# Optimization experiments

Hardware: AMD Instinct MI355X
Metric: run time of the kernel (lower is better)

The kernel has to match this reference:

```python
import jax, jax.numpy as jnp
import numpy as np

B, T, H, I = 128, 1024, 512, 64
DT, TAU, NOISE_VAR = 1.0, 10.0, 0.1


def setup_inputs() -> dict:
    key = jax.random.key(0)
    k1, k2, k3, k4 = jax.random.split(key, 4)
    x = jax.random.normal(k1, (B, T, I), dtype=jnp.float32)
    # W_in: rows have unit-ish norm in the original init; normal/sqrt(I) is equivalent scale
    W_in = jax.random.normal(k2, (H, I), dtype=jnp.float32) / np.float32(np.sqrt(I))
    # W_hidden: randn/sqrt(H) then spectral-radius normalized; /sqrt(H) gives radius ~1
    W_hidden = jax.random.normal(k3, (H, H), dtype=jnp.float32) / np.float32(np.sqrt(H))
    # noise drawn inside forward in the original; materialized here: N(0, noise_var)
    sigma = jax.random.normal(k4, (H, T, B), dtype=jnp.float32) * np.float32(NOISE_VAR)
    h0 = jnp.zeros((H, B), dtype=jnp.float32)
    return {"x": x, "W_in": W_in, "W_hidden": W_hidden, "sigma": sigma, "h0": h0}


def reference(x, W_in, W_hidden, sigma, h0):
    c1 = jnp.float32(1.0 - DT / TAU)
    c2 = jnp.float32(DT / TAU)
    # precomputed input projection: [T, H, B] (scan carries over leading T axis)
    w_input = jnp.einsum("hi,bti->thb", W_in, x)
    sig = jnp.transpose(sigma, (1, 0, 2))  # [T, H, B]

    def step(h, inp):
        w_in_t, s_t = inp
        w_h = W_hidden @ jax.nn.sigmoid(h)          # [H, B]
        h_new = c1 * h + c2 * (w_in_t + w_h + s_t)  # leaky integration
        return h_new, h_new.T                        # emit [B, H]

    h_last, out_tbh = jax.lax.scan(step, h0, (w_input, sig))
    out = jnp.transpose(out_tbh, (1, 0, 2))  # [B, T, H]
    return out, h_last
```

## Files before the change

### kernel.cpp

```cpp
#include <hip/hip_runtime.h>
#include <stdint.h>

#define B_  128
#define T_  1024
#define H_  512
#define I_  64
#define TB_ 131072

typedef _Float16 half2_t __attribute__((ext_vector_type(2)));

union U32H2 { uint32_t u; half2_t h; };
union U16H  { uint16_t u; _Float16 h; };

static __device__ __forceinline__ half2_t u2h(uint32_t u){ U32H2 x; x.u=u; return x.h; }
static __device__ __forceinline__ uint32_t h2u(half2_t h){ U32H2 x; x.h=h; return x.u; }

#if defined(__has_builtin)
#if __has_builtin(__builtin_amdgcn_fdot2)
#define HAVE_FDOT2 1
#endif
#endif

static __device__ __forceinline__ float fdot2f(half2_t a, half2_t b, float c){
#ifdef HAVE_FDOT2
    return __builtin_amdgcn_fdot2(a, b, c, false);
#else
    return c + (float)a[0]*(float)b[0] + (float)a[1]*(float)b[1];
#endif
}

__global__ __launch_bounds__(256) void k_wingemm(const float* __restrict__ x,
                                                 const float* __restrict__ Win,
                                                 uint32_t* __restrict__ r2)
{
    __shared__ float As[128*65];
    __shared__ float Ws[64*65];
    const int t   = blockIdx.x;
    const int j0  = blockIdx.y * 64;
    const int tid = threadIdx.x;

#pragma unroll
    for (int k = 0; k < 8; k++){
        int qid = k*256 + tid;
        int row = qid >> 4;
        int qq  = qid & 15;
        float4 v = *(const float4*)(x + ((size_t)row*T_ + t)*I_ + qq*4);
        float* d = As + row*65 + qq*4;
        d[0]=v.x; d[1]=v.y; d[2]=v.z; d[3]=v.w;
    }
#pragma unroll
    for (int k = 0; k < 4; k++){
        int qid = k*256 + tid;
        int row = qid >> 4;
        int qq  = qid & 15;
        float4 v = *(const float4*)(Win + (size_t)(j0+row)*I_ + qq*4);
        float* d = Ws + row*65 + qq*4;
        d[0]=v.x; d[1]=v.y; d[2]=v.z; d[3]=v.w;
    }
    __syncthreads();

    const int tj = tid & 15;
    const int tb = tid >> 4;

    float acc[8][2][2];
#pragma unroll
    for (int bb=0; bb<8; bb++)
#pragma unroll
        for (int jj=0; jj<2; jj++){ acc[bb][jj][0]=0.f; acc[bb][jj][1]=0.f; }

#pragma unroll 4
    for (int i = 0; i < 64; i++){
        float a[8];
#pragma unroll
        for (int bb=0; bb<8; bb++) a[bb] = As[(tb + 16*bb)*65 + i];
        float wv[2][2];
#pragma unroll
        for (int jj=0; jj<2; jj++){
            wv[jj][0] = Ws[(2*tj + 32*jj    )*65 + i];
            wv[jj][1] = Ws[(2*tj + 32*jj + 1)*65 + i];
        }
#pragma unroll
        for (int bb=0; bb<8; bb++)
#pragma unroll
            for (int jj=0; jj<2; jj++){
                acc[bb][jj][0] += a[bb]*wv[jj][0];
                acc[bb][jj][1] += a[bb]*wv[jj][1];
            }
    }

#pragma unroll
    for (int bb=0; bb<8; bb++){
        int mi = t*128 + tb + 16*bb;
#pragma unroll
        for (int jj=0; jj<2; jj++){
            half2_t hv; hv[0]=(_Float16)acc[bb][jj][0]; hv[1]=(_Float16)acc[bb][jj][1];
            r2[(size_t)mi*256 + (j0>>1) + tj + 16*jj] = h2u(hv);
        }
    }
}

static __device__ __forceinline__ uint32_t addpair(uint32_t u, float a0, float a1){
    half2_t h = u2h(u);
    half2_t o; o[0]=(_Float16)((float)h[0] + a0); o[1]=(_Float16)((float)h[1] + a1);
    return h2u(o);
}

__global__ __launch_bounds__(256) void k_addsig(const float* __restrict__ sigma,
                                                uint32_t* __restrict__ r2)
{
    __shared__ float Ss[64*256];
    const int mi0 = blockIdx.x * 256;
    const int j0  = blockIdx.y * 64;
    const int tid = threadIdx.x;

#pragma unroll
    for (int k = 0; k < 16; k++){
        int qid = k*256 + tid;
        int row = qid >> 6;
        int qq  = qid & 63;
        float4 v = *(const float4*)(sigma + (size_t)(j0+row)*TB_ + mi0 + qq*4);
        *(float4*)(Ss + row*256 + qq*4) = v;
    }
    __syncthreads();

    const int mi = mi0 + tid;
    uint32_t* rr = r2 + (size_t)mi*256 + (j0>>1);
#pragma unroll
    for (int k = 0; k < 8; k++){
        uint4 q = *(uint4*)(rr + 4*k);
        q.x = addpair(q.x, Ss[(8*k+0)*256+tid], Ss[(8*k+1)*256+tid]);
        q.y = addpair(q.y, Ss[(8*k+2)*256+tid], Ss[(8*k+3)*256+tid]);
        q.z = addpair(q.z, Ss[(8*k+4)*256+tid], Ss[(8*k+5)*256+tid]);
        q.w = addpair(q.w, Ss[(8*k+6)*256+tid], Ss[(8*k+7)*256+tid]);
        *(uint4*)(rr + 4*k) = q;
    }
}

__global__ __launch_bounds__(512, 2) void k_rnn(const float* __restrict__ Wh,
                                                const float* __restrict__ Win,
                                                const float* __restrict__ x,
                                                const float* __restrict__ sigma,
                                                const float* __restrict__ h0,
                                                const uint16_t* __restrict__ r16,
                                                float* __restrict__ out,
                                                int use_r)
{
    extern __shared__ char smem[];
    uint32_t*  WL  = (uint32_t*)smem;
    float*     par = (float*)(smem + 131072);
    _Float16*  sb  = (_Float16*)(smem + 147456);

    const int b = blockIdx.x;
    const int t = threadIdx.x;
    const int w = t >> 6;
    const int l = t & 63;
    const int j = t;
    const int phase = (l & 15) << 2;

    half2_t wreg[6][32];
#pragma unroll
    for (int m = 0; m < 8; m++){
        const int row = l + 64*m;
        const float4* wr = (const float4*)(Wh + (size_t)row*H_ + (w << 6));
#pragma unroll
        for (int q = 0; q < 16; q++){
            float4 v = wr[q];
            half2_t a; a[0]=(_Float16)v.x; a[1]=(_Float16)v.y;
            half2_t c; c[0]=(_Float16)v.z; c[1]=(_Float16)v.w;
            int pp = 2*q;
            if (m < 6){
                wreg[m][pp]   = a;
                wreg[m][pp+1] = c;
            } else {
                int base = (m-6)*32;
                WL[t*64 + ((base + pp     + phase) & 63)] = h2u(a);
                WL[t*64 + ((base + pp + 1 + phase) & 63)] = h2u(c);
            }
        }
    }

    float h = h0[(size_t)j*B_ + b];
    const uint32_t* WLt = WL + t*64;
    const uint32_t* sbu = (const uint32_t*)sb;
    float* outp = out + (size_t)b*T_*H_ + j;
    const uint16_t* rp = r16 + (size_t)b*H_ + j;

    for (int ts = 0; ts < T_; ts++){
        uint16_t ru = 0;
        if (use_r) ru = rp[(size_t)ts * 65536];

        float e = __expf(-h);
        float s = 1.0f / (1.0f + e);
        sb[j] = (_Float16)s;
        __syncthreads();

        float p[8];
#pragma unroll
        for (int m = 0; m < 8; m++) p[m] = 0.f;

#pragma unroll
        for (int c = 0; c < 8; c++){
            uint4 sq = *(const uint4*)(sbu + (w << 5) + (c << 2));
            half2_t s0=u2h(sq.x), s1=u2h(sq.y), s2=u2h(sq.z), s3=u2h(sq.w);
            uint4 q6 = *(const uint4*)(WLt + ((4*c      + phase) & 63));
            uint4 q7 = *(const uint4*)(WLt + ((32 + 4*c + phase) & 63));
#pragma unroll
            for (int m = 0; m < 6; m++){
                p[m] = fdot2f(wreg[m][4*c+0], s0, p[m]);
                p[m] = fdot2f(wreg[m][4*c+1], s1, p[m]);
                p[m] = fdot2f(wreg[m][4*c+2], s2, p[m]);
                p[m] = fdot2f(wreg[m][4*c+3], s3, p[m]);
            }
            p[6] = fdot2f(u2h(q6.x), s0, p[6]);
            p[6] = fdot2f(u2h(q6.y), s1, p[6]);
            p[6] = fdot2f(u2h(q6.z), s2, p[6]);
            p[6] = fdot2f(u2h(q6.w), s3, p[6]);
            p[7] = fdot2f(u2h(q7.x), s0, p[7]);
            p[7] = fdot2f(u2h(q7.y), s1, p[7]);
            p[7] = fdot2f(u2h(q7.z), s2, p[7]);
            p[7] = fdot2f(u2h(q7.w), s3, p[7]);
        }

#pragma unroll
        for (int m = 0; m < 8; m++) par[(w << 9) + l + (m << 6)] = p[m];
        __syncthreads();

        float P = par[j] + par[j+512] + par[j+1024] + par[j+1536]
                + par[j+2048] + par[j+2560] + par[j+3072] + par[j+3584];

        float rv;
        if (use_r){
            U16H cv; cv.u = ru;
            rv = (float)cv.h;
        } else {
            float acc = 0.f;
            const float4* wir = (const float4*)(Win + (size_t)j*I_);
            const float4* xr  = (const float4*)(x + ((size_t)b*T_ + ts)*I_);
#pragma unroll
            for (int q = 0; q < 16; q++){
                float4 a = wir[q]; float4 xx = xr[q];
                acc += a.x*xx.x + a.y*xx.y + a.z*xx.z + a.w*xx.w;
            }
            rv = acc + sigma[((size_t)j << 17) + (ts << 7) + b];
        }

        h = 0.9f*h + 0.1f*(P + rv);
        outp[(size_t)ts * H_] = h;
    }

    out[(size_t)B_*T_*H_ + (size_t)j*B_ + b] = h;
}

extern "C" void kernel_launch(void* const* d_in, const int* in_sizes, int n_in,
                              void* d_out, int out_size, void* d_ws, size_t ws_size,
                              hipStream_t stream)
{
    const float* x     = (const float*)d_in[0];
    const float* Win   = (const float*)d_in[1];
    const float* Wh    = (const float*)d_in[2];
    const float* sigma = (const float*)d_in[3];
    const float* h0    = (const float*)d_in[4];
    float* out = (float*)d_out;

    const size_t r_bytes = (size_t)TB_ * H_ * 2;
    const int use_r = (ws_size >= r_bytes) ? 1 : 0;

    if (use_r){
        k_wingemm<<<dim3(T_, 8), 256, 0, stream>>>(x, Win, (uint32_t*)d_ws);
        k_addsig <<<dim3(TB_/256, 8), 256, 0, stream>>>(sigma, (uint32_t*)d_ws);
    }

    const int lds_bytes = 131072 + 16384 + 1024;
    (void)hipFuncSetAttribute((const void*)k_rnn,
                              hipFuncAttributeMaxDynamicSharedMemorySize, lds_bytes);
    k_rnn<<<B_, 512, lds_bytes, stream>>>(Wh, Win, x, sigma, h0,
                                          (const uint16_t*)d_ws, out, use_r);
}
```

Before: 2.525 ms.

## Fuse input projection and noise add into one prep kernel; vectorize RNN weight registers

Replaces the separate W_in GEMM kernel and sigma-add kernel with a single k_prep kernel per timestep. It computes all 512 hidden outputs in two 256-wide chunks, adds sigma from global memory and writes the fp16 result once, which removes a full read-modify-write pass over the workspace. The recurrent kernel's register-resident weights move from a 2D half2 array to six 32-wide uint32 vectors and use waves_per_eu attributes, to encourage the compiler to keep them in VGPRs without spilling. The sigma reads in k_prep are strided per thread, which may coalesce poorly, and the RNN loop itself stays the dominant serial cost.

Result: slower. 3.504 ms (+38.7%).

```diff
diff --git a/kernel.cpp b/kernel.cpp
--- a/kernel.cpp
+++ b/kernel.cpp
@@ -8,6 +8,7 @@
 #define TB_ 131072
 
 typedef _Float16 half2_t __attribute__((ext_vector_type(2)));
+typedef uint32_t u32v32  __attribute__((ext_vector_type(32)));
 
 union U32H2 { uint32_t u; half2_t h; };
 union U16H  { uint16_t u; _Float16 h; };
@@ -29,121 +30,96 @@
 #endif
 }
 
-__global__ __launch_bounds__(256) void k_wingemm(const float* __restrict__ x,
-                                                 const float* __restrict__ Win,
-                                                 uint32_t* __restrict__ r2)
+#define PADA 68
+
+__global__ __attribute__((amdgpu_flat_work_group_size(512,512)))
+void k_prep(const float* __restrict__ x, const float* __restrict__ Win,
+            const float* __restrict__ sigma, uint32_t* __restrict__ r2)
 {
-    __shared__ float As[128*65];
-    __shared__ float Ws[64*65];
+    extern __shared__ float smemA[];
+    float* As = smemA;
+    float* Ws = smemA + 128*PADA;
+
     const int t   = blockIdx.x;
-    const int j0  = blockIdx.y * 64;
     const int tid = threadIdx.x;
-
-#pragma unroll
-    for (int k = 0; k < 8; k++){
-        int qid = k*256 + tid;
-        int row = qid >> 4;
-        int qq  = qid & 15;
+    const int tm  = tid & 31;
+    const int tg  = tid >> 5;
+
+#pragma unroll
+    for (int k = 0; k < 4; k++){
+        int qid = k*512 + tid;
+        int row = qid >> 4, qq = qid & 15;
         float4 v = *(const float4*)(x + ((size_t)row*T_ + t)*I_ + qq*4);
-        float* d = As + row*65 + qq*4;
-        d[0]=v.x; d[1]=v.y; d[2]=v.z; d[3]=v.w;
-    }
-#pragma unroll
-    for (int k = 0; k < 4; k++){
-        int qid = k*256 + tid;
-        int row = qid >> 4;
-        int qq  = qid & 15;
-        float4 v = *(const float4*)(Win + (size_t)(j0+row)*I_ + qq*4);
-        float* d = Ws + row*65 + qq*4;
-        d[0]=v.x; d[1]=v.y; d[2]=v.z; d[3]=v.w;
-    }
-    __syncthreads();
-
-    const int tj = tid & 15;
-    const int tb = tid >> 4;
-
-    float acc[8][2][2];
-#pragma unroll
-    for (int bb=0; bb<8; bb++)
-#pragma unroll
-        for (int jj=0; jj<2; jj++){ acc[bb][jj][0]=0.f; acc[bb][jj][1]=0.f; }
-
-#pragma unroll 4
-    for (int i = 0; i < 64; i++){
-        float a[8];
-#pragma unroll
-        for (int bb=0; bb<8; bb++) a[bb] = As[(tb + 16*bb)*65 + i];
-        float wv[2][2];
-#pragma unroll
-        for (int jj=0; jj<2; jj++){
-            wv[jj][0] = Ws[(2*tj + 32*jj    )*65 + i];
-            wv[jj][1] = Ws[(2*tj + 32*jj + 1)*65 + i];
-        }
-#pragma unroll
-        for (int bb=0; bb<8; bb++)
-#pragma unroll
-            for (int jj=0; jj<2; jj++){
-                acc[bb][jj][0] += a[bb]*wv[jj][0];
-                acc[bb][jj][1] += a[bb]*wv[jj][1];
+        *(float4*)(As + row*PADA + qq*4) = v;
+    }
+
+    for (int ch = 0; ch < 2; ch++){
+        const int j0 = ch*256;
+        __syncthreads();
+#pragma unroll
+        for (int k = 0; k < 8; k++){
+            int qid = k*512 + tid;
+            int row = qid >> 4, qq = qid & 15;
+            float4 v = *(const float4*)(Win + (size_t)(j0+row)*I_ + qq*4);
+            *(float4*)(Ws + row*PADA + qq*4) = v;
+        }
+        __syncthreads();
+
+        float acc[4][16];
+#pragma unroll
+        for (int rr=0;rr<4;rr++)
+#pragma unroll
+            for (int jj=0;jj<16;jj++) acc[rr][jj] = 0.f;
+
+#pragma unroll
+        for (int ic = 0; ic < 16; ic++){
+            float4 a4[4];
+#pragma unroll
+            for (int rr=0;rr<4;rr++)
+                a4[rr] = *(const float4*)(As + (size_t)(tm+32*rr)*PADA + ic*4);
+#pragma unroll
+            for (int jj=0;jj<16;jj++){
+                float4 wv = *(const float4*)(Ws + (size_t)(tg*16+jj)*PADA + ic*4);
+#pragma unroll
+                for (int rr=0;rr<4;rr++)
+                    acc[rr][jj] += a4[rr].x*wv.x + a4[rr].y*wv.y
+                                 + a4[rr].z*wv.z + a4[rr].w*wv.w;
             }
-    }
-
-#pragma unroll
-    for (int bb=0; bb<8; bb++){
-        int mi = t*128 + tb + 16*bb;
-#pragma unroll
-        for (int jj=0; jj<2; jj++){
-            half2_t hv; hv[0]=(_Float16)acc[bb][jj][0]; hv[1]=(_Float16)acc[bb][jj][1];
-            r2[(size_t)mi*256 + (j0>>1) + tj + 16*jj] = h2u(hv);
-        }
-    }
-}
-
-static __device__ __forceinline__ uint32_t addpair(uint32_t u, float a0, float a1){
-    half2_t h = u2h(u);
-    half2_t o; o[0]=(_Float16)((float)h[0] + a0); o[1]=(_Float16)((float)h[1] + a1);
-    return h2u(o);
-}
-
-__global__ __launch_bounds__(256) void k_addsig(const float* __restrict__ sigma,
-                                                uint32_t* __restrict__ r2)
-{
-    __shared__ float Ss[64*256];
-    const int mi0 = blockIdx.x * 256;
-    const int j0  = blockIdx.y * 64;
-    const int tid = threadIdx.x;
-
-#pragma unroll
-    for (int k = 0; k < 16; k++){
-        int qid = k*256 + tid;
-        int row = qid >> 6;
-        int qq  = qid & 63;
-        float4 v = *(const float4*)(sigma + (size_t)(j0+row)*TB_ + mi0 + qq*4);
-        *(float4*)(Ss + row*256 + qq*4) = v;
-    }
-    __syncthreads();
-
-    const int mi = mi0 + tid;
-    uint32_t* rr = r2 + (size_t)mi*256 + (j0>>1);
-#pragma unroll
-    for (int k = 0; k < 8; k++){
-        uint4 q = *(uint4*)(rr + 4*k);
-        q.x = addpair(q.x, Ss[(8*k+0)*256+tid], Ss[(8*k+1)*256+tid]);
-        q.y = addpair(q.y, Ss[(8*k+2)*256+tid], Ss[(8*k+3)*256+tid]);
-        q.z = addpair(q.z, Ss[(8*k+4)*256+tid], Ss[(8*k+5)*256+tid]);
-        q.w = addpair(q.w, Ss[(8*k+6)*256+tid], Ss[(8*k+7)*256+tid]);
-        *(uint4*)(rr + 4*k) = q;
-    }
-}
-
-__global__ __launch_bounds__(512, 2) void k_rnn(const float* __restrict__ Wh,
-                                                const float* __restrict__ Win,
-                                                const float* __restrict__ x,
-                                                const float* __restrict__ sigma,
-                                                const float* __restrict__ h0,
-                                                const uint16_t* __restrict__ r16,
-                                                float* __restrict__ out,
-                                                int use_r)
+        }
+
+#pragma unroll
+        for (int rr=0; rr<4; rr++){
+            const size_t mi = (size_t)t*128 + tm + 32*rr;
+            const float* sp = sigma + (size_t)(j0 + tg*16)*TB_ + mi;
+            uint32_t ou[8];
+#pragma unroll
+            for (int k2=0;k2<8;k2++){
+                float sA = sp[(size_t)(2*k2  )*TB_];
+                float sB = sp[(size_t)(2*k2+1)*TB_];
+                half2_t hv;
+                hv[0] = (_Float16)(acc[rr][2*k2  ] + sA);
+                hv[1] = (_Float16)(acc[rr][2*k2+1] + sB);
+                ou[k2] = h2u(hv);
+            }
+            uint32_t* dst = r2 + mi*256 + (j0>>1) + tg*8;
+            uint4 q0 = make_uint4(ou[0],ou[1],ou[2],ou[3]);
+            uint4 q1 = make_uint4(ou[4],ou[5],ou[6],ou[7]);
+            *(uint4*)(dst)     = q0;
+            *(uint4*)(dst + 4) = q1;
+        }
+    }
+}
+
+__global__ __attribute__((amdgpu_flat_work_group_size(512,512)))
+           __attribute__((amdgpu_waves_per_eu(2,2)))
+void k_rnn(const float* __restrict__ Wh,
+           const float* __restrict__ Win,
+           const float* __restrict__ x,
+           const float* __restrict__ sigma,
+           const float* __restrict__ h0,
+           const uint16_t* __restrict__ r16,
+           float* __restrict__ out,
+           int use_r)
 {
     extern __shared__ char smem[];
     uint32_t*  WL  = (uint32_t*)smem;
@@ -157,25 +133,32 @@
     const int j = t;
     const int phase = (l & 15) << 2;
 
-    half2_t wreg[6][32];
-#pragma unroll
-    for (int m = 0; m < 8; m++){
-        const int row = l + 64*m;
-        const float4* wr = (const float4*)(Wh + (size_t)row*H_ + (w << 6));
+    u32v32 w0, w1, w2, w3, w4, w5;
+#define LOADR(VM, M) { \
+    const float4* wr = (const float4*)(Wh + (size_t)(l + 64*(M))*H_ + (w << 6)); \
+    _Pragma("unroll") \
+    for (int q = 0; q < 16; q++){ \
+        float4 v = wr[q]; \
+        half2_t a;  a[0]=(_Float16)v.x;  a[1]=(_Float16)v.y; \
+        half2_t c2; c2[0]=(_Float16)v.z; c2[1]=(_Float16)v.w; \
+        VM[2*q]   = h2u(a); \
+        VM[2*q+1] = h2u(c2); \
+    } }
+    LOADR(w0, 0) LOADR(w1, 1) LOADR(w2, 2)
+    LOADR(w3, 3) LOADR(w4, 4) LOADR(w5, 5)
+#undef LOADR
+
+#pragma unroll
+    for (int m = 6; m < 8; m++){
+        const float4* wr = (const float4*)(Wh + (size_t)(l + 64*m)*H_ + (w << 6));
 #pragma unroll
         for (int q = 0; q < 16; q++){
             float4 v = wr[q];
-            half2_t a; a[0]=(_Float16)v.x; a[1]=(_Float16)v.y;
-            half2_t c; c[0]=(_Float16)v.z; c[1]=(_Float16)v.w;
-            int pp = 2*q;
-            if (m < 6){
-                wreg[m][pp]   = a;
-                wreg[m][pp+1] = c;
-            } else {
-                int base = (m-6)*32;
-                WL[t*64 + ((base + pp     + phase) & 63)] = h2u(a);
-                WL[t*64 + ((base + pp + 1 + phase) & 63)] = h2u(c);
-            }
+            half2_t a;  a[0]=(_Float16)v.x;  a[1]=(_Float16)v.y;
+            half2_t c2; c2[0]=(_Float16)v.z; c2[1]=(_Float16)v.w;
+            int base = (m-6)*32, pp = 2*q;
+            WL[t*64 + ((base + pp     + phase) & 63)] = h2u(a);
+            WL[t*64 + ((base + pp + 1 + phase) & 63)] = h2u(c2);
         }
     }
 
@@ -199,18 +182,19 @@
         for (int m = 0; m < 8; m++) p[m] = 0.f;
 
 #pragma unroll
-        for (int c = 0; c < 8; c++){
-            uint4 sq = *(const uint4*)(sbu + (w << 5) + (c << 2));
+        for (int cc = 0; cc < 8; cc++){
+            uint4 sq = *(const uint4*)(sbu + (w << 5) + (cc << 2));
             half2_t s0=u2h(sq.x), s1=u2h(sq.y), s2=u2h(sq.z), s3=u2h(sq.w);
-            uint4 q6 = *(const uint4*)(WLt + ((4*c      + phase) & 63));
-            uint4 q7 = *(const uint4*)(WLt + ((32 + 4*c + phase) & 63));
-#pragma unroll
-            for (int m = 0; m < 6; m++){
-                p[m] = fdot2f(wreg[m][4*c+0], s0, p[m]);
-                p[m] = fdot2f(wreg[m][4*c+1], s1, p[m]);
-                p[m] = fdot2f(wreg[m][4*c+2], s2, p[m]);
-                p[m] = fdot2f(wreg[m][4*c+3], s3, p[m]);
-            }
+            uint4 q6 = *(const uint4*)(WLt + ((4*cc      + phase) & 63));
+            uint4 q7 = *(const uint4*)(WLt + ((32 + 4*cc + phase) & 63));
+#define DOT4(VM, PM) \
+            p[PM] = fdot2f(u2h(VM[4*cc+0]), s0, p[PM]); \
+            p[PM] = fdot2f(u2h(VM[4*cc+1]), s1, p[PM]); \
+            p[PM] = fdot2f(u2h(VM[4*cc+2]), s2, p[PM]); \
+            p[PM] = fdot2f(u2h(VM[4*cc+3]), s3, p[PM]);
+            DOT4(w0, 0) DOT4(w1, 1) DOT4(w2, 2)
+            DOT4(w3, 3) DOT4(w4, 4) DOT4(w5, 5)
+#undef DOT4
             p[6] = fdot2f(u2h(q6.x), s0, p[6]);
             p[6] = fdot2f(u2h(q6.y), s1, p[6]);
             p[6] = fdot2f(u2h(q6.z), s2, p[6]);
@@ -266,8 +250,10 @@
     const int use_r = (ws_size >= r_bytes) ? 1 : 0;
 
     if (use_r){
-        k_wingemm<<<dim3(T_, 8), 256, 0, stream>>>(x, Win, (uint32_t*)d_ws);
-        k_addsig <<<dim3(TB_/256, 8), 256, 0, stream>>>(sigma, (uint32_t*)d_ws);
+        const int prep_lds = (128 + 256) * PADA * 4;
+        (void)hipFuncSetAttribute((const void*)k_prep,
+                                  hipFuncAttributeMaxDynamicSharedMemorySize, prep_lds);
+        k_prep<<<T_, 512, prep_lds, stream>>>(x, Win, sigma, (uint32_t*)d_ws);
     }
 
     const int lds_bytes = 131072 + 16384 + 1024;
```
